# Kernel tuning notes

Measured on AMD Instinct MI355X. Metric: run time of the kernel, lower is better.

The kernel has to match this reference:

```python
import jax, jax.numpy as jnp
import numpy as np

D_MODEL = 1024
NUM_HEADS = 16
D_K = D_MODEL // NUM_HEADS
B, S = 2, 2048


def setup_inputs() -> dict:
    key = jax.random.key(0)
    ks = jax.random.split(key, 11)
    sc = 1.0 / np.sqrt(D_MODEL)
    inp = {
        "query": jax.random.normal(ks[0], (B, S, D_MODEL), jnp.float32),
        "key": jax.random.normal(ks[1], (B, S, D_MODEL), jnp.float32),
        "value": jax.random.normal(ks[2], (B, S, D_MODEL), jnp.float32),
        "Wq": jax.random.normal(ks[3], (D_MODEL, D_MODEL), jnp.float32) * sc,
        "bq": jax.random.normal(ks[4], (D_MODEL,), jnp.float32) * sc,
        "Wk": jax.random.normal(ks[5], (D_MODEL, D_MODEL), jnp.float32) * sc,
        "bk": jax.random.normal(ks[6], (D_MODEL,), jnp.float32) * sc,
        "Wv": jax.random.normal(ks[7], (D_MODEL, D_MODEL), jnp.float32) * sc,
        "bv": jax.random.normal(ks[8], (D_MODEL,), jnp.float32) * sc,
        "Wo": jax.random.normal(ks[9], (D_MODEL, D_MODEL), jnp.float32) * sc,
        "bo": jax.random.normal(ks[10], (D_MODEL,), jnp.float32) * sc,
    }
    return inp


def reference(query, key, value, Wq, bq, Wk, bk, Wv, bv, Wo, bo):
    b = query.shape[0]
    # Linear projections (torch Linear: x @ W.T + b), W is [out, in]
    Q = query @ Wq.T + bq
    K = key @ Wk.T + bk
    V = value @ Wv.T + bv
    # [B, S, D] -> [B, H, S, d_k]
    Q = Q.reshape(b, -1, NUM_HEADS, D_K).transpose(0, 2, 1, 3)
    K = K.reshape(b, -1, NUM_HEADS, D_K).transpose(0, 2, 1, 3)
    V = V.reshape(b, -1, NUM_HEADS, D_K).transpose(0, 2, 1, 3)
    # Scaled dot-product attention (mask=None, dropout inactive in eval)
    scores = jnp.einsum("bhqd,bhkd->bhqk", Q, K) / jnp.sqrt(jnp.float32(D_K))
    attn = jax.nn.softmax(scores, axis=-1)
    out = jnp.einsum("bhqk,bhkd->bhqd", attn, V)
    # [B, H, S, d_k] -> [B, S, D]
    out = out.transpose(0, 2, 1, 3).reshape(b, -1, D_MODEL)
    return out @ Wo.T + bo
```

## Files before the change

kernel.cpp:

```cpp
#include <hip/hip_runtime.h>

typedef __bf16 bf16x8 __attribute__((ext_vector_type(8)));
typedef __bf16 bf16x4 __attribute__((ext_vector_type(4)));
typedef float f32x4 __attribute__((ext_vector_type(4)));

#define D_MODEL 1024
#define NUM_HEADS 16
#define DK 64
#define BATCH 2
#define SEQ 2048
#define M_ROWS (BATCH*SEQ)

#define QSCALE 0.18033688011112042f

#define GLOAD_LDS16(gp, lp) __builtin_amdgcn_global_load_lds( \
    (__attribute__((address_space(1))) void*)(gp), \
    (__attribute__((address_space(3))) void*)(lp), 16, 0, 0)

__global__ __launch_bounds__(256) void cvt3(
    const float* __restrict__ s0, const float* __restrict__ s1,
    const float* __restrict__ s2, __bf16* __restrict__ dst, int n)
{
  const float* s = blockIdx.y == 0 ? s0 : (blockIdx.y == 1 ? s1 : s2);
  __bf16* d = dst + (size_t)blockIdx.y * n;
  int i = (blockIdx.x * 256 + threadIdx.x) * 8;
  if (i >= n) return;
  float4 a = *(const float4*)(s + i);
  float4 b = *(const float4*)(s + i + 4);
  bf16x8 o;
  o[0] = (__bf16)a.x; o[1] = (__bf16)a.y; o[2] = (__bf16)a.z; o[3] = (__bf16)a.w;
  o[4] = (__bf16)b.x; o[5] = (__bf16)b.y; o[6] = (__bf16)b.z; o[7] = (__bf16)b.w;
  *(bf16x8*)(d + i) = o;
}

__global__ __launch_bounds__(256) void cvt4(
    const float* __restrict__ s0, const float* __restrict__ s1,
    const float* __restrict__ s2, const float* __restrict__ s3,
    __bf16* __restrict__ dst, int n)
{
  const float* s = blockIdx.y == 0 ? s0 : (blockIdx.y == 1 ? s1 :
                   (blockIdx.y == 2 ? s2 : s3));
  __bf16* d = dst + (size_t)blockIdx.y * n;
  int i = (blockIdx.x * 256 + threadIdx.x) * 8;
  if (i >= n) return;
  float4 a = *(const float4*)(s + i);
  float4 b = *(const float4*)(s + i + 4);
  bf16x8 o;
  o[0] = (__bf16)a.x; o[1] = (__bf16)a.y; o[2] = (__bf16)a.z; o[3] = (__bf16)a.w;
  o[4] = (__bf16)b.x; o[5] = (__bf16)b.y; o[6] = (__bf16)b.z; o[7] = (__bf16)b.w;
  *(bf16x8*)(d + i) = o;
}

template <typename OutT>
__device__ __forceinline__ void gemm_body(
    const __bf16* __restrict__ A, const __bf16* __restrict__ W,
    const float* __restrict__ bias, OutT* __restrict__ C,
    int M, int N, int K, int m0, int n0, float scale)
{
  __shared__ __align__(16) __bf16 sA[128*64];
  __shared__ __align__(16) __bf16 sB[128*64];
  const int tid  = threadIdx.x;
  const int wave = tid >> 6;
  const int lane = tid & 63;
  const int l16  = lane & 15;
  const int quad = lane >> 4;
  const int wm = (wave >> 1) * 64;
  const int wn = (wave & 1) * 64;

  f32x4 acc[4][4] = {};

  const int gsw = (((tid & 7) ^ ((tid >> 3) & 7))) * 8;
  long aoff[4], boff[4];
#pragma unroll
  for (int i = 0; i < 4; i++) {
    int row = (i * 256 + tid) >> 3;
    aoff[i] = (long)(m0 + row) * K + gsw;
    boff[i] = (long)(n0 + row) * K + gsw;
  }
  const int rsw = l16 & 7;

  for (int k0 = 0; k0 < K; k0 += 64) {
    __syncthreads();
#pragma unroll
    for (int i = 0; i < 4; i++) {
      GLOAD_LDS16(A + aoff[i] + k0, (char*)sA + i * 4096 + wave * 1024);
      GLOAD_LDS16(W + boff[i] + k0, (char*)sB + i * 4096 + wave * 1024);
    }
    __syncthreads();
#pragma unroll
    for (int ks = 0; ks < 2; ks++) {
      bf16x8 af[4], bf[4];
#pragma unroll
      for (int i = 0; i < 4; i++)
        af[i] = *(const bf16x8*)&sA[(wm + i * 16 + l16) * 64 + ((ks * 4 + quad) ^ rsw) * 8];
#pragma unroll
      for (int j = 0; j < 4; j++)
        bf[j] = *(const bf16x8*)&sB[(wn + j * 16 + l16) * 64 + ((ks * 4 + quad) ^ rsw) * 8];
#pragma unroll
      for (int i = 0; i < 4; i++)
#pragma unroll
        for (int j = 0; j < 4; j++)
          acc[i][j] = __builtin_amdgcn_mfma_f32_16x16x32_bf16(af[i], bf[j], acc[i][j], 0, 0, 0);
    }
  }

#pragma unroll
  for (int j = 0; j < 4; j++) {
    int col = n0 + wn + j * 16 + l16;
    float bv = bias[col];
#pragma unroll
    for (int i = 0; i < 4; i++) {
      long row0 = m0 + wm + i * 16 + quad * 4;
#pragma unroll
      for (int r = 0; r < 4; r++)
        C[(row0 + r) * N + col] = (OutT)((acc[i][j][r] + bv) * scale);
    }
  }
}

__global__ __launch_bounds__(256) void gemm_qkv(
    const __bf16* __restrict__ Abase, const __bf16* __restrict__ Wbase,
    const float* __restrict__ b0, const float* __restrict__ b1,
    const float* __restrict__ b2, __bf16* __restrict__ Cbase)
{
  int z = blockIdx.z;
  const __bf16* A = Abase + (size_t)z * M_ROWS * D_MODEL;
  const __bf16* W = Wbase + (size_t)z * D_MODEL * D_MODEL;
  const float* bias = z == 0 ? b0 : (z == 1 ? b1 : b2);
  float scale = z == 0 ? QSCALE : 1.0f;
  __bf16* C = Cbase + (size_t)z * M_ROWS * D_MODEL;
  gemm_body<__bf16>(A, W, bias, C, M_ROWS, D_MODEL, D_MODEL,
                    blockIdx.y * 128, blockIdx.x * 128, scale);
}

__global__ __launch_bounds__(256) void gemm_out(
    const __bf16* __restrict__ A, const __bf16* __restrict__ W,
    const float* __restrict__ bias, float* __restrict__ C)
{
  gemm_body<float>(A, W, bias, C, M_ROWS, D_MODEL, D_MODEL,
                   blockIdx.y * 128, blockIdx.x * 128, 1.0f);
}

__global__ __launch_bounds__(512) void attn_kernel(
    const __bf16* __restrict__ Q, const __bf16* __restrict__ K,
    const __bf16* __restrict__ V, __bf16* __restrict__ O)
{
  constexpr int SV_LD = 136;

  __shared__ __align__(16) __bf16 sK[128 * 64];
  __shared__ __align__(16) __bf16 sVt[DK * SV_LD];

  const int tid  = threadIdx.x;
  const int wave = tid >> 6;
  const int lane = tid & 63;
  const int l16  = lane & 15;
  const int quad = lane >> 4;

  const int bh = blockIdx.y;
  const int b  = bh >> 4, h = bh & (NUM_HEADS - 1);
  const int q0 = blockIdx.x * 128;
  const long base = (long)b * SEQ * D_MODEL + h * DK;

  const __bf16* qrow = Q + base + (long)(q0 + wave * 16 + l16) * D_MODEL + quad * 8;
  const bf16x8 aq0 = *(const bf16x8*)(qrow);
  const bf16x8 aq1 = *(const bf16x8*)(qrow + 32);

  const int gsw = (((tid & 7) ^ ((tid >> 3) & 7))) * 8;
  const __bf16* kp[2];
#pragma unroll
  for (int i = 0; i < 2; i++)
    kp[i] = K + base + (long)((i * 512 + tid) >> 3) * D_MODEL + gsw;
  const int rsw = l16 & 7;

  const __bf16* vp0 = V + base + (long)(2 * lane) * D_MODEL + wave * 8;
  const int k5 = (2 * lane) & 31;
  const int pos5 = ((k5 & 12) << 1) | ((k5 & 16) >> 2) | (k5 & 3);
  const int vcol = (lane >> 4) * 16 + (pos5 >> 1);

  uint4 kr0 = *(const uint4*)(kp[0]);
  uint4 kr1 = *(const uint4*)(kp[1]);
  uint4 vr0 = *(const uint4*)(vp0);
  uint4 vr1 = *(const uint4*)(vp0 + D_MODEL);

  f32x4 lacc = {};
  f32x4 o[4] = {};

  for (int t = 0; t < SEQ / 128; t++) {
    __syncthreads();
    *(uint4*)((char*)sK + tid * 16) = kr0;
    *(uint4*)((char*)sK + 8192 + tid * 16) = kr1;
    {
      const ushort* e0 = (const ushort*)&vr0;
      const ushort* e1 = (const ushort*)&vr1;
      uint* dst = (uint*)sVt;
#pragma unroll
      for (int j = 0; j < 8; j++)
        dst[(wave * 8 + j) * (SV_LD / 2) + vcol] = (uint)e0[j] | ((uint)e1[j] << 16);
    }
    if (t + 1 < SEQ / 128) {
      long adv = (long)(t + 1) * 128 * D_MODEL;
      kr0 = *(const uint4*)(kp[0] + adv);
      kr1 = *(const uint4*)(kp[1] + adv);
      vr0 = *(const uint4*)(vp0 + adv);
      vr1 = *(const uint4*)(vp0 + adv + D_MODEL);
    }
    __syncthreads();

#pragma unroll
    for (int kt = 0; kt < 4; kt++) {
      bf16x8 af;
#pragma unroll
      for (int hh = 0; hh < 2; hh++) {
        int nt = 2 * kt + hh;
        bf16x8 b0 = *(const bf16x8*)&sK[(nt * 16 + l16) * 64 + (quad ^ rsw) * 8];
        bf16x8 b1 = *(const bf16x8*)&sK[(nt * 16 + l16) * 64 + ((4 + quad) ^ rsw) * 8];
        f32x4 z = {};
        __builtin_amdgcn_s_setprio(1);
        z = __builtin_amdgcn_mfma_f32_16x16x32_bf16(b0, aq0, z, 0, 0, 0);
        z = __builtin_amdgcn_mfma_f32_16x16x32_bf16(b1, aq1, z, 0, 0, 0);
        __builtin_amdgcn_s_setprio(0);
        f32x4 p;
#pragma unroll
        for (int r = 0; r < 4; r++) p[r] = exp2f(z[r]);
        lacc += p;
#pragma unroll
        for (int r = 0; r < 4; r++) af[hh * 4 + r] = (__bf16)p[r];
      }
      __builtin_amdgcn_s_setprio(1);
#pragma unroll
      for (int dt = 0; dt < 4; dt++) {
        bf16x8 bv = *(const bf16x8*)&sVt[(dt * 16 + l16) * SV_LD + kt * 32 + quad * 8];
        o[dt] = __builtin_amdgcn_mfma_f32_16x16x32_bf16(af, bv, o[dt], 0, 0, 0);
      }
      __builtin_amdgcn_s_setprio(0);
    }
  }

  float ls = lacc[0] + lacc[1] + lacc[2] + lacc[3];
  ls += __shfl_xor(ls, 16, 64);
  ls += __shfl_xor(ls, 32, 64);
  float rls[4];
#pragma unroll
  for (int r = 0; r < 4; r++)
    rls[r] = 1.0f / __shfl(ls, quad * 4 + r, 64);

#pragma unroll
  for (int dt = 0; dt < 4; dt++) {
#pragma unroll
    for (int r = 0; r < 4; r++) {
      int s = q0 + wave * 16 + quad * 4 + r;
      int d = dt * 16 + l16;
      O[base + (long)s * D_MODEL + d] = (__bf16)(o[dt][r] * rls[r]);
    }
  }
}

extern "C" void kernel_launch(void* const* d_in, const int* in_sizes, int n_in,
                              void* d_out, int out_size, void* d_ws, size_t ws_size,
                              hipStream_t stream) {
  const float* q  = (const float*)d_in[0];
  const float* k  = (const float*)d_in[1];
  const float* v  = (const float*)d_in[2];
  const float* Wq = (const float*)d_in[3];
  const float* bq = (const float*)d_in[4];
  const float* Wk = (const float*)d_in[5];
  const float* bk = (const float*)d_in[6];
  const float* Wv = (const float*)d_in[7];
  const float* bv = (const float*)d_in[8];
  const float* Wo = (const float*)d_in[9];
  const float* bo = (const float*)d_in[10];
  float* out = (float*)d_out;

  const size_t ACT = (size_t)M_ROWS * D_MODEL;
  const size_t WSZ = (size_t)D_MODEL * D_MODEL;
  __bf16* qc  = (__bf16*)d_ws;
  __bf16* Wqc = qc + 3 * ACT;
  __bf16* wsQ = Wqc + 4 * WSZ;
  __bf16* wsAo = qc;

  dim3 blk(256);
  cvt3<<<dim3(ACT / 2048, 3), blk, 0, stream>>>(q, k, v, qc, (int)ACT);
  cvt4<<<dim3(WSZ / 2048, 4), blk, 0, stream>>>(Wq, Wk, Wv, Wo, Wqc, (int)WSZ);

  gemm_qkv<<<dim3(D_MODEL / 128, M_ROWS / 128, 3), blk, 0, stream>>>(
      qc, Wqc, bq, bk, bv, wsQ);

  attn_kernel<<<dim3(SEQ / 128, BATCH * NUM_HEADS), dim3(512), 0, stream>>>(
      wsQ, wsQ + ACT, wsQ + 2 * ACT, wsAo);

  gemm_out<<<dim3(D_MODEL / 128, M_ROWS / 128), blk, 0, stream>>>(
      wsAo, Wqc + 3 * WSZ, bo, out);
}
```

Measured before the change: 249.2 us.

## Halve attention block to 4 waves each owning 32 query rows; merge convert kernels

The attention kernel now runs 256 threads per block, and each wave handles two 16-row query groups. Every K and V fragment read from LDS therefore feeds twice as many MFMAs, and each thread loads twice as much of each K/V tile from global memory. The separate activation and weight fp32-to-bf16 conversion kernels are merged into one launch, removing a kernel launch. The trade-off is higher register pressure from the doubled accumulators and fewer waves per block to hide latency.

```diff
diff --git a/kernel.cpp b/kernel.cpp
--- a/kernel.cpp
+++ b/kernel.cpp
@@ -17,38 +17,34 @@
     (__attribute__((address_space(1))) void*)(gp), \
     (__attribute__((address_space(3))) void*)(lp), 16, 0, 0)
 
-__global__ __launch_bounds__(256) void cvt3(
-    const float* __restrict__ s0, const float* __restrict__ s1,
-    const float* __restrict__ s2, __bf16* __restrict__ dst, int n)
-{
-  const float* s = blockIdx.y == 0 ? s0 : (blockIdx.y == 1 ? s1 : s2);
-  __bf16* d = dst + (size_t)blockIdx.y * n;
-  int i = (blockIdx.x * 256 + threadIdx.x) * 8;
-  if (i >= n) return;
-  float4 a = *(const float4*)(s + i);
-  float4 b = *(const float4*)(s + i + 4);
+#define ACT ((size_t)M_ROWS * D_MODEL)
+#define WSZ ((size_t)D_MODEL * D_MODEL)
+
+__global__ __launch_bounds__(256) void cvt_all(
+    const float* __restrict__ q, const float* __restrict__ k,
+    const float* __restrict__ v, const float* __restrict__ wq,
+    const float* __restrict__ wk, const float* __restrict__ wv,
+    const float* __restrict__ wo, __bf16* __restrict__ dst)
+{
+  size_t e = ((size_t)blockIdx.x * 256 + threadIdx.x) * 8;
+  const float* s;
+  size_t off;
+  if (e < 3 * ACT) {
+    int t = (int)(e >> 22);
+    s = t == 0 ? q : (t == 1 ? k : v);
+    off = e & (ACT - 1);
+  } else {
+    size_t e2 = e - 3 * ACT;
+    int t = (int)(e2 >> 20);
+    s = t == 0 ? wq : (t == 1 ? wk : (t == 2 ? wv : wo));
+    off = e2 & (WSZ - 1);
+  }
+  float4 a = *(const float4*)(s + off);
+  float4 b = *(const float4*)(s + off + 4);
   bf16x8 o;
   o[0] = (__bf16)a.x; o[1] = (__bf16)a.y; o[2] = (__bf16)a.z; o[3] = (__bf16)a.w;
   o[4] = (__bf16)b.x; o[5] = (__bf16)b.y; o[6] = (__bf16)b.z; o[7] = (__bf16)b.w;
-  *(bf16x8*)(d + i) = o;
-}
-
-__global__ __launch_bounds__(256) void cvt4(
-    const float* __restrict__ s0, const float* __restrict__ s1,
-    const float* __restrict__ s2, const float* __restrict__ s3,
-    __bf16* __restrict__ dst, int n)
-{
-  const float* s = blockIdx.y == 0 ? s0 : (blockIdx.y == 1 ? s1 :
-                   (blockIdx.y == 2 ? s2 : s3));
-  __bf16* d = dst + (size_t)blockIdx.y * n;
-  int i = (blockIdx.x * 256 + threadIdx.x) * 8;
-  if (i >= n) return;
-  float4 a = *(const float4*)(s + i);
-  float4 b = *(const float4*)(s + i + 4);
-  bf16x8 o;
-  o[0] = (__bf16)a.x; o[1] = (__bf16)a.y; o[2] = (__bf16)a.z; o[3] = (__bf16)a.w;
-  o[4] = (__bf16)b.x; o[5] = (__bf16)b.y; o[6] = (__bf16)b.z; o[7] = (__bf16)b.w;
-  *(bf16x8*)(d + i) = o;
+  *(bf16x8*)(dst + e) = o;
 }
 
 template <typename OutT>
@@ -141,7 +137,7 @@
                    blockIdx.y * 128, blockIdx.x * 128, 1.0f);
 }
 
-__global__ __launch_bounds__(512) void attn_kernel(
+__global__ __launch_bounds__(256) void attn_kernel(
     const __bf16* __restrict__ Q, const __bf16* __restrict__ K,
     const __bf16* __restrict__ V, __bf16* __restrict__ O)
 {
@@ -161,96 +157,123 @@
   const int q0 = blockIdx.x * 128;
   const long base = (long)b * SEQ * D_MODEL + h * DK;
 
-  const __bf16* qrow = Q + base + (long)(q0 + wave * 16 + l16) * D_MODEL + quad * 8;
-  const bf16x8 aq0 = *(const bf16x8*)(qrow);
-  const bf16x8 aq1 = *(const bf16x8*)(qrow + 32);
+  bf16x8 aq[2][2];
+#pragma unroll
+  for (int g = 0; g < 2; g++) {
+    const __bf16* qrow =
+        Q + base + (long)(q0 + wave * 32 + g * 16 + l16) * D_MODEL + quad * 8;
+    aq[g][0] = *(const bf16x8*)(qrow);
+    aq[g][1] = *(const bf16x8*)(qrow + 32);
+  }
 
   const int gsw = (((tid & 7) ^ ((tid >> 3) & 7))) * 8;
-  const __bf16* kp[2];
-#pragma unroll
-  for (int i = 0; i < 2; i++)
-    kp[i] = K + base + (long)((i * 512 + tid) >> 3) * D_MODEL + gsw;
+  const __bf16* kp[4];
+#pragma unroll
+  for (int i = 0; i < 4; i++)
+    kp[i] = K + base + (long)((i * 256 + tid) >> 3) * D_MODEL + gsw;
   const int rsw = l16 & 7;
 
-  const __bf16* vp0 = V + base + (long)(2 * lane) * D_MODEL + wave * 8;
+  const __bf16* vp0 = V + base + (long)(2 * lane) * D_MODEL + wave * 16;
   const int k5 = (2 * lane) & 31;
   const int pos5 = ((k5 & 12) << 1) | ((k5 & 16) >> 2) | (k5 & 3);
   const int vcol = (lane >> 4) * 16 + (pos5 >> 1);
 
-  uint4 kr0 = *(const uint4*)(kp[0]);
-  uint4 kr1 = *(const uint4*)(kp[1]);
-  uint4 vr0 = *(const uint4*)(vp0);
-  uint4 vr1 = *(const uint4*)(vp0 + D_MODEL);
-
-  f32x4 lacc = {};
-  f32x4 o[4] = {};
+  uint4 kr[4], vr[4];
+#pragma unroll
+  for (int i = 0; i < 4; i++) kr[i] = *(const uint4*)(kp[i]);
+  vr[0] = *(const uint4*)(vp0);
+  vr[1] = *(const uint4*)(vp0 + 8);
+  vr[2] = *(const uint4*)(vp0 + D_MODEL);
+  vr[3] = *(const uint4*)(vp0 + D_MODEL + 8);
+
+  f32x4 lacc[2] = {};
+  f32x4 o[2][4] = {};
 
   for (int t = 0; t < SEQ / 128; t++) {
     __syncthreads();
-    *(uint4*)((char*)sK + tid * 16) = kr0;
-    *(uint4*)((char*)sK + 8192 + tid * 16) = kr1;
+#pragma unroll
+    for (int i = 0; i < 4; i++)
+      *(uint4*)((char*)sK + i * 4096 + tid * 16) = kr[i];
     {
-      const ushort* e0 = (const ushort*)&vr0;
-      const ushort* e1 = (const ushort*)&vr1;
+      const ushort* e0 = (const ushort*)&vr[0];
+      const ushort* e1 = (const ushort*)&vr[1];
+      const ushort* e2 = (const ushort*)&vr[2];
+      const ushort* e3 = (const ushort*)&vr[3];
       uint* dst = (uint*)sVt;
 #pragma unroll
-      for (int j = 0; j < 8; j++)
-        dst[(wave * 8 + j) * (SV_LD / 2) + vcol] = (uint)e0[j] | ((uint)e1[j] << 16);
+      for (int j = 0; j < 8; j++) {
+        dst[(wave * 16 + j) * (SV_LD / 2) + vcol] =
+            (uint)e0[j] | ((uint)e2[j] << 16);
+        dst[(wave * 16 + 8 + j) * (SV_LD / 2) + vcol] =
+            (uint)e1[j] | ((uint)e3[j] << 16);
+      }
     }
     if (t + 1 < SEQ / 128) {
       long adv = (long)(t + 1) * 128 * D_MODEL;
-      kr0 = *(const uint4*)(kp[0] + adv);
-      kr1 = *(const uint4*)(kp[1] + adv);
-      vr0 = *(const uint4*)(vp0 + adv);
-      vr1 = *(const uint4*)(vp0 + adv + D_MODEL);
+#pragma unroll
+      for (int i = 0; i < 4; i++) kr[i] = *(const uint4*)(kp[i] + adv);
+      vr[0] = *(const uint4*)(vp0 + adv);
+      vr[1] = *(const uint4*)(vp0 + adv + 8);
+      vr[2] = *(const uint4*)(vp0 + adv + D_MODEL);
+      vr[3] = *(const uint4*)(vp0 + adv + D_MODEL + 8);
     }
     __syncthreads();
 
 #pragma unroll
     for (int kt = 0; kt < 4; kt++) {
-      bf16x8 af;
+      bf16x8 af0, af1;
 #pragma unroll
       for (int hh = 0; hh < 2; hh++) {
         int nt = 2 * kt + hh;
         bf16x8 b0 = *(const bf16x8*)&sK[(nt * 16 + l16) * 64 + (quad ^ rsw) * 8];
         bf16x8 b1 = *(const bf16x8*)&sK[(nt * 16 + l16) * 64 + ((4 + quad) ^ rsw) * 8];
-        f32x4 z = {};
+        f32x4 z0 = {}, z1 = {};
         __builtin_amdgcn_s_setprio(1);
-        z = __builtin_amdgcn_mfma_f32_16x16x32_bf16(b0, aq0, z, 0, 0, 0);
-        z = __builtin_amdgcn_mfma_f32_16x16x32_bf16(b1, aq1, z, 0, 0, 0);
+        z0 = __builtin_amdgcn_mfma_f32_16x16x32_bf16(b0, aq[0][0], z0, 0, 0, 0);
+        z0 = __builtin_amdgcn_mfma_f32_16x16x32_bf16(b1, aq[0][1], z0, 0, 0, 0);
+        z1 = __builtin_amdgcn_mfma_f32_16x16x32_bf16(b0, aq[1][0], z1, 0, 0, 0);
+        z1 = __builtin_amdgcn_mfma_f32_16x16x32_bf16(b1, aq[1][1], z1, 0, 0, 0);
         __builtin_amdgcn_s_setprio(0);
-        f32x4 p;
-#pragma unroll
-        for (int r = 0; r < 4; r++) p[r] = exp2f(z[r]);
-        lacc += p;
-#pragma unroll
-        for (int r = 0; r < 4; r++) af[hh * 4 + r] = (__bf16)p[r];
+        f32x4 p0, p1;
+#pragma unroll
+        for (int r = 0; r < 4; r++) p0[r] = exp2f(z0[r]);
+#pragma unroll
+        for (int r = 0; r < 4; r++) p1[r] = exp2f(z1[r]);
+        lacc[0] += p0;
+        lacc[1] += p1;
+#pragma unroll
+        for (int r = 0; r < 4; r++) af0[hh * 4 + r] = (__bf16)p0[r];
+#pragma unroll
+        for (int r = 0; r < 4; r++) af1[hh * 4 + r] = (__bf16)p1[r];
       }
       __builtin_amdgcn_s_setprio(1);
 #pragma unroll
       for (int dt = 0; dt < 4; dt++) {
         bf16x8 bv = *(const bf16x8*)&sVt[(dt * 16 + l16) * SV_LD + kt * 32 + quad * 8];
-        o[dt] = __builtin_amdgcn_mfma_f32_16x16x32_bf16(af, bv, o[dt], 0, 0, 0);
+        o[0][dt] = __builtin_amdgcn_mfma_f32_16x16x32_bf16(af0, bv, o[0][dt], 0, 0, 0);
+        o[1][dt] = __builtin_amdgcn_mfma_f32_16x16x32_bf16(af1, bv, o[1][dt], 0, 0, 0);
       }
       __builtin_amdgcn_s_setprio(0);
     }
   }
 
-  float ls = lacc[0] + lacc[1] + lacc[2] + lacc[3];
-  ls += __shfl_xor(ls, 16, 64);
-  ls += __shfl_xor(ls, 32, 64);
-  float rls[4];
-#pragma unroll
-  for (int r = 0; r < 4; r++)
-    rls[r] = 1.0f / __shfl(ls, quad * 4 + r, 64);
-
-#pragma unroll
-  for (int dt = 0; dt < 4; dt++) {
-#pragma unroll
-    for (int r = 0; r < 4; r++) {
-      int s = q0 + wave * 16 + quad * 4 + r;
-      int d = dt * 16 + l16;
-      O[base + (long)s * D_MODEL + d] = (__bf16)(o[dt][r] * rls[r]);
+#pragma unroll
+  for (int g = 0; g < 2; g++) {
+    float ls = lacc[g][0] + lacc[g][1] + lacc[g][2] + lacc[g][3];
+    ls += __shfl_xor(ls, 16, 64);
+    ls += __shfl_xor(ls, 32, 64);
+    float rls[4];
+#pragma unroll
+    for (int r = 0; r < 4; r++)
+      rls[r] = 1.0f / __shfl(ls, quad * 4 + r, 64);
+#pragma unroll
+    for (int dt = 0; dt < 4; dt++) {
+#pragma unroll
+      for (int r = 0; r < 4; r++) {
+        int s = q0 + wave * 32 + g * 16 + quad * 4 + r;
+        int d = dt * 16 + l16;
+        O[base + (long)s * D_MODEL + d] = (__bf16)(o[g][dt][r] * rls[r]);
+      }
     }
   }
 }
@@ -271,21 +294,19 @@
   const float* bo = (const float*)d_in[10];
   float* out = (float*)d_out;
 
-  const size_t ACT = (size_t)M_ROWS * D_MODEL;
-  const size_t WSZ = (size_t)D_MODEL * D_MODEL;
   __bf16* qc  = (__bf16*)d_ws;
   __bf16* Wqc = qc + 3 * ACT;
   __bf16* wsQ = Wqc + 4 * WSZ;
   __bf16* wsAo = qc;
 
   dim3 blk(256);
-  cvt3<<<dim3(ACT / 2048, 3), blk, 0, stream>>>(q, k, v, qc, (int)ACT);
-  cvt4<<<dim3(WSZ / 2048, 4), blk, 0, stream>>>(Wq, Wk, Wv, Wo, Wqc, (int)WSZ);
+  cvt_all<<<dim3((3 * ACT + 4 * WSZ) / 2048), blk, 0, stream>>>(
+      q, k, v, Wq, Wk, Wv, Wo, qc);
 
   gemm_qkv<<<dim3(D_MODEL / 128, M_ROWS / 128, 3), blk, 0, stream>>>(
       qc, Wqc, bq, bk, bv, wsQ);
 
-  attn_kernel<<<dim3(SEQ / 128, BATCH * NUM_HEADS), dim3(512), 0, stream>>>(
+  attn_kernel<<<dim3(SEQ / 128, BATCH * NUM_HEADS), dim3(256), 0, stream>>>(
       wsQ, wsQ + ACT, wsQ + 2 * ACT, wsAo);
 
   gemm_out<<<dim3(D_MODEL / 128, M_ROWS / 128), blk, 0, stream>>>(
```

Result: slower. 270.3 us (+8.5%).

## Split attention key tiles across wave pairs, merge conversion kernels, use fast exp2

Applied to the files above, without the earlier changes.

The attention kernel now processes 64 queries per block instead of 128. The two wave groups each handle half of every 128-key tile, and their partial outputs and row sums are combined through shared memory at the end. This doubles the grid to give more parallelism and shortens per-wave MFMA chains, at the cost of K/V tiles being reloaded by twice as many blocks plus an extra reduction step. The separate fp32-to-bf16 conversion kernels are merged into one launch, and exp2f is swapped for the hardware exp2 builtin when available.

```diff
diff --git a/kernel.cpp b/kernel.cpp
--- a/kernel.cpp
+++ b/kernel.cpp
@@ -13,42 +13,47 @@
 
 #define QSCALE 0.18033688011112042f
 
+#if defined(__has_builtin)
+#if __has_builtin(__builtin_amdgcn_exp2f)
+#define EXP2(x) __builtin_amdgcn_exp2f(x)
+#endif
+#endif
+#ifndef EXP2
+#define EXP2(x) exp2f(x)
+#endif
+
 #define GLOAD_LDS16(gp, lp) __builtin_amdgcn_global_load_lds( \
     (__attribute__((address_space(1))) void*)(gp), \
     (__attribute__((address_space(3))) void*)(lp), 16, 0, 0)
 
-__global__ __launch_bounds__(256) void cvt3(
-    const float* __restrict__ s0, const float* __restrict__ s1,
-    const float* __restrict__ s2, __bf16* __restrict__ dst, int n)
-{
-  const float* s = blockIdx.y == 0 ? s0 : (blockIdx.y == 1 ? s1 : s2);
-  __bf16* d = dst + (size_t)blockIdx.y * n;
-  int i = (blockIdx.x * 256 + threadIdx.x) * 8;
-  if (i >= n) return;
-  float4 a = *(const float4*)(s + i);
-  float4 b = *(const float4*)(s + i + 4);
+#define ACT ((size_t)M_ROWS * D_MODEL)
+#define WSZ ((size_t)D_MODEL * D_MODEL)
+
+__global__ __launch_bounds__(256) void cvt_all(
+    const float* __restrict__ q, const float* __restrict__ k,
+    const float* __restrict__ v, const float* __restrict__ wq,
+    const float* __restrict__ wk, const float* __restrict__ wv,
+    const float* __restrict__ wo, __bf16* __restrict__ dst)
+{
+  size_t e = ((size_t)blockIdx.x * 256 + threadIdx.x) * 8;
+  const float* s;
+  size_t off;
+  if (e < 3 * ACT) {
+    int t = (int)(e >> 22);
+    s = t == 0 ? q : (t == 1 ? k : v);
+    off = e & (ACT - 1);
+  } else {
+    size_t e2 = e - 3 * ACT;
+    int t = (int)(e2 >> 20);
+    s = t == 0 ? wq : (t == 1 ? wk : (t == 2 ? wv : wo));
+    off = e2 & (WSZ - 1);
+  }
+  float4 a = *(const float4*)(s + off);
+  float4 b = *(const float4*)(s + off + 4);
   bf16x8 o;
   o[0] = (__bf16)a.x; o[1] = (__bf16)a.y; o[2] = (__bf16)a.z; o[3] = (__bf16)a.w;
   o[4] = (__bf16)b.x; o[5] = (__bf16)b.y; o[6] = (__bf16)b.z; o[7] = (__bf16)b.w;
-  *(bf16x8*)(d + i) = o;
-}
-
-__global__ __launch_bounds__(256) void cvt4(
-    const float* __restrict__ s0, const float* __restrict__ s1,
-    const float* __restrict__ s2, const float* __restrict__ s3,
-    __bf16* __restrict__ dst, int n)
-{
-  const float* s = blockIdx.y == 0 ? s0 : (blockIdx.y == 1 ? s1 :
-                   (blockIdx.y == 2 ? s2 : s3));
-  __bf16* d = dst + (size_t)blockIdx.y * n;
-  int i = (blockIdx.x * 256 + threadIdx.x) * 8;
-  if (i >= n) return;
-  float4 a = *(const float4*)(s + i);
-  float4 b = *(const float4*)(s + i + 4);
-  bf16x8 o;
-  o[0] = (__bf16)a.x; o[1] = (__bf16)a.y; o[2] = (__bf16)a.z; o[3] = (__bf16)a.w;
-  o[4] = (__bf16)b.x; o[5] = (__bf16)b.y; o[6] = (__bf16)b.z; o[7] = (__bf16)b.w;
-  *(bf16x8*)(d + i) = o;
+  *(bf16x8*)(dst + e) = o;
 }
 
 template <typename OutT>
@@ -149,19 +154,22 @@
 
   __shared__ __align__(16) __bf16 sK[128 * 64];
   __shared__ __align__(16) __bf16 sVt[DK * SV_LD];
+  __shared__ float lsbuf[8][16];
 
   const int tid  = threadIdx.x;
   const int wave = tid >> 6;
+  const int g    = wave & 3;
+  const int kh   = wave >> 2;
   const int lane = tid & 63;
   const int l16  = lane & 15;
   const int quad = lane >> 4;
 
   const int bh = blockIdx.y;
   const int b  = bh >> 4, h = bh & (NUM_HEADS - 1);
-  const int q0 = blockIdx.x * 128;
+  const int q0 = blockIdx.x * 64;
   const long base = (long)b * SEQ * D_MODEL + h * DK;
 
-  const __bf16* qrow = Q + base + (long)(q0 + wave * 16 + l16) * D_MODEL + quad * 8;
+  const __bf16* qrow = Q + base + (long)(q0 + g * 16 + l16) * D_MODEL + quad * 8;
   const bf16x8 aq0 = *(const bf16x8*)(qrow);
   const bf16x8 aq1 = *(const bf16x8*)(qrow + 32);
 
@@ -207,11 +215,12 @@
     __syncthreads();
 
 #pragma unroll
-    for (int kt = 0; kt < 4; kt++) {
+    for (int kl = 0; kl < 2; kl++) {
+      const int kt = kh * 2 + kl;
       bf16x8 af;
 #pragma unroll
       for (int hh = 0; hh < 2; hh++) {
-        int nt = 2 * kt + hh;
+        int nt = kt * 2 + hh;
         bf16x8 b0 = *(const bf16x8*)&sK[(nt * 16 + l16) * 64 + (quad ^ rsw) * 8];
         bf16x8 b1 = *(const bf16x8*)&sK[(nt * 16 + l16) * 64 + ((4 + quad) ^ rsw) * 8];
         f32x4 z = {};
@@ -221,7 +230,7 @@
         __builtin_amdgcn_s_setprio(0);
         f32x4 p;
 #pragma unroll
-        for (int r = 0; r < 4; r++) p[r] = exp2f(z[r]);
+        for (int r = 0; r < 4; r++) p[r] = EXP2(z[r]);
         lacc += p;
 #pragma unroll
         for (int r = 0; r < 4; r++) af[hh * 4 + r] = (__bf16)p[r];
@@ -239,18 +248,31 @@
   float ls = lacc[0] + lacc[1] + lacc[2] + lacc[3];
   ls += __shfl_xor(ls, 16, 64);
   ls += __shfl_xor(ls, 32, 64);
-  float rls[4];
-#pragma unroll
-  for (int r = 0; r < 4; r++)
-    rls[r] = 1.0f / __shfl(ls, quad * 4 + r, 64);
-
-#pragma unroll
-  for (int dt = 0; dt < 4; dt++) {
-#pragma unroll
-    for (int r = 0; r < 4; r++) {
-      int s = q0 + wave * 16 + quad * 4 + r;
-      int d = dt * 16 + l16;
-      O[base + (long)s * D_MODEL + d] = (__bf16)(o[dt][r] * rls[r]);
+
+  __syncthreads();
+  if (quad == 0) lsbuf[wave][l16] = ls;
+  f32x4* scr = (f32x4*)sK;
+  if (kh == 1) {
+#pragma unroll
+    for (int dt = 0; dt < 4; dt++)
+      scr[dt * 256 + g * 64 + lane] = o[dt];
+  }
+  __syncthreads();
+  if (kh == 0) {
+    float lst = lsbuf[g][l16] + lsbuf[4 + g][l16];
+    float rls[4];
+#pragma unroll
+    for (int r = 0; r < 4; r++)
+      rls[r] = 1.0f / __shfl(lst, quad * 4 + r, 64);
+#pragma unroll
+    for (int dt = 0; dt < 4; dt++) {
+      f32x4 oo = o[dt] + scr[dt * 256 + g * 64 + lane];
+#pragma unroll
+      for (int r = 0; r < 4; r++) {
+        int s = q0 + g * 16 + quad * 4 + r;
+        int d = dt * 16 + l16;
+        O[base + (long)s * D_MODEL + d] = (__bf16)(oo[r] * rls[r]);
+      }
     }
   }
 }
@@ -271,21 +293,19 @@
   const float* bo = (const float*)d_in[10];
   float* out = (float*)d_out;
 
-  const size_t ACT = (size_t)M_ROWS * D_MODEL;
-  const size_t WSZ = (size_t)D_MODEL * D_MODEL;
   __bf16* qc  = (__bf16*)d_ws;
   __bf16* Wqc = qc + 3 * ACT;
   __bf16* wsQ = Wqc + 4 * WSZ;
   __bf16* wsAo = qc;
 
   dim3 blk(256);
-  cvt3<<<dim3(ACT / 2048, 3), blk, 0, stream>>>(q, k, v, qc, (int)ACT);
-  cvt4<<<dim3(WSZ / 2048, 4), blk, 0, stream>>>(Wq, Wk, Wv, Wo, Wqc, (int)WSZ);
+  cvt_all<<<dim3((3 * ACT + 4 * WSZ) / 2048), blk, 0, stream>>>(
+      q, k, v, Wq, Wk, Wv, Wo, qc);
 
   gemm_qkv<<<dim3(D_MODEL / 128, M_ROWS / 128, 3), blk, 0, stream>>>(
       qc, Wqc, bq, bk, bv, wsQ);
 
-  attn_kernel<<<dim3(SEQ / 128, BATCH * NUM_HEADS), dim3(512), 0, stream>>>(
+  attn_kernel<<<dim3(SEQ / 64, BATCH * NUM_HEADS), dim3(512), 0, stream>>>(
       wsQ, wsQ + ACT, wsQ + 2 * ACT, wsAo);
 
   gemm_out<<<dim3(D_MODEL / 128, M_ROWS / 128), blk, 0, stream>>>(
```

Measured after the change: 246.7 us. About the same (-1.0%).
